# Kernel optimization log

Measured on AMD Instinct MI355X. Metric: run time of the kernel, lower is better.

## Reference

```python
import jax, jax.numpy as jnp
import numpy as np

EPS = 1e-05


def setup_inputs() -> dict:
    key = jax.random.key(0)
    k1, k2, k3, k4 = jax.random.split(key, 4)
    B, C, L, S = 32, 256, 8192, 4
    x = jax.random.normal(k1, (B, C, L), dtype=jnp.float32)
    style_ids = jax.random.randint(k2, (B,), 0, S)
    # per-style affine params, as in nn.InstanceNorm1d(affine=True):
    # torch initializes weight=1, bias=0; use small perturbations so styles differ
    weight = jnp.ones((S, C), dtype=jnp.float32) + 0.1 * jax.random.normal(k3, (S, C), dtype=jnp.float32)
    bias = 0.1 * jax.random.normal(k4, (S, C), dtype=jnp.float32)
    return {"x": x, "weight": weight, "bias": bias, "style_ids": style_ids}


def reference(x, weight, bias, style_ids):
    # x: [B, C, L]; instance norm: normalize each (b, c) row over L (biased var)
    mean = jnp.mean(x, axis=-1, keepdims=True)            # [B, C, 1]
    var = jnp.mean(jnp.square(x - mean), axis=-1, keepdims=True)  # biased, [B, C, 1]
    x_hat = (x - mean) * jax.lax.rsqrt(var + EPS)
    # gather per-sample style affine params: [B, C]
    w = weight[style_ids]
    b = bias[style_ids]
    return x_hat * w[:, :, None] + b[:, :, None]
```

## Files before the change

kernel.cpp:

```cpp
#include <hip/hip_runtime.h>
#include <math.h>


constexpr int L_LEN  = 8192;
constexpr int NTHR   = 512;
constexpr int VPT    = L_LEN / (NTHR * 4);
constexpr int NWAVE  = NTHR / 64;
constexpr float EPS_ = 1e-5f;

typedef float f32x4 __attribute__((ext_vector_type(4)));

__global__ __launch_bounds__(NTHR) void cin1d_kernel(
    const float* __restrict__ x,
    const float* __restrict__ weight,
    const float* __restrict__ bias,
    const int*   __restrict__ style_ids,
    float* __restrict__ out,
    int C)
{
    const int row = blockIdx.x;
    const int b   = row / C;
    const int c   = row - b * C;
    const int t   = threadIdx.x;

    const int   sid = style_ids[b];
    const float w   = weight[sid * C + c];
    const float bb  = bias[sid * C + c];

    const f32x4* __restrict__ xr   = reinterpret_cast<const f32x4*>(x + (size_t)row * L_LEN);
    f32x4* __restrict__       outr = reinterpret_cast<f32x4*>(out + (size_t)row * L_LEN);

    f32x4 v[VPT];
    float sum = 0.f, sq = 0.f;
#pragma unroll
    for (int i = 0; i < VPT; ++i) {
        v[i] = __builtin_nontemporal_load(&xr[t + i * NTHR]);
        sum += v[i].x + v[i].y + v[i].z + v[i].w;
        sq  += v[i].x * v[i].x + v[i].y * v[i].y + v[i].z * v[i].z + v[i].w * v[i].w;
    }

#pragma unroll
    for (int off = 32; off > 0; off >>= 1) {
        sum += __shfl_xor(sum, off, 64);
        sq  += __shfl_xor(sq,  off, 64);
    }

    __shared__ float s_sum[NWAVE];
    __shared__ float s_sq[NWAVE];
    const int wave = t >> 6;
    const int lane = t & 63;
    if (lane == 0) { s_sum[wave] = sum; s_sq[wave] = sq; }
    __syncthreads();

    float ts = 0.f, tq = 0.f;
#pragma unroll
    for (int wv = 0; wv < NWAVE; ++wv) { ts += s_sum[wv]; tq += s_sq[wv]; }
    const float inv_n = 1.0f / (float)L_LEN;
    const float mean  = ts * inv_n;
    const float var   = tq * inv_n - mean * mean;
    const float rstd  = rsqrtf(var + EPS_);
    const float scale = w * rstd;
    const float shift = bb - mean * scale;

#pragma unroll
    for (int i = 0; i < VPT; ++i) {
        f32x4 o;
        o.x = v[i].x * scale + shift;
        o.y = v[i].y * scale + shift;
        o.z = v[i].z * scale + shift;
        o.w = v[i].w * scale + shift;
        __builtin_nontemporal_store(o, &outr[t + i * NTHR]);
    }
}

extern "C" void kernel_launch(void* const* d_in, const int* in_sizes, int n_in,
                              void* d_out, int out_size, void* d_ws, size_t ws_size,
                              hipStream_t stream) {
    const float* x      = (const float*)d_in[0];
    const float* weight = (const float*)d_in[1];
    const float* bias   = (const float*)d_in[2];
    const int*   sids   = (const int*)d_in[3];
    float*       out    = (float*)d_out;

    const int B = in_sizes[3];
    const int C = in_sizes[0] / (B * L_LEN);
    const int rows = B * C;

    cin1d_kernel<<<rows, NTHR, 0, stream>>>(x, weight, bias, sids, out, C);
}
```

Baseline: 96.49 us.

## Process four rows per block with double-buffered prefetch of next row

Each block now handles four consecutive rows instead of one, and loads the next row into a second register buffer while reducing and writing the current row. This aims to hide global load latency behind the reduction, sync and store phases and to cut per-block launch overhead. In exchange it doubles register use per thread, which may lower occupancy, and it reduces the block count fourfold. It assumes C is divisible by 4.

```diff
diff --git a/kernel.cpp b/kernel.cpp
--- a/kernel.cpp
+++ b/kernel.cpp
@@ -2,10 +2,11 @@
 #include <math.h>
 
 
-constexpr int L_LEN  = 8192;
-constexpr int NTHR   = 512;
-constexpr int VPT    = L_LEN / (NTHR * 4);
-constexpr int NWAVE  = NTHR / 64;
+constexpr int L_LEN = 8192;
+constexpr int NTHR  = 512;
+constexpr int VPT   = L_LEN / (NTHR * 4);
+constexpr int NWAVE = NTHR / 64;
+constexpr int RPB   = 4;
 constexpr float EPS_ = 1e-5f;
 
 typedef float f32x4 __attribute__((ext_vector_type(4)));
@@ -18,58 +19,81 @@
     float* __restrict__ out,
     int C)
 {
-    const int row = blockIdx.x;
-    const int b   = row / C;
-    const int c   = row - b * C;
-    const int t   = threadIdx.x;
+    const int row0 = blockIdx.x * RPB;
+    const int b    = row0 / C;
+    const int c0   = row0 - b * C;
+    const int t    = threadIdx.x;
+    const int wave = t >> 6;
+    const int lane = t & 63;
 
-    const int   sid = style_ids[b];
-    const float w   = weight[sid * C + c];
-    const float bb  = bias[sid * C + c];
-
-    const f32x4* __restrict__ xr   = reinterpret_cast<const f32x4*>(x + (size_t)row * L_LEN);
-    f32x4* __restrict__       outr = reinterpret_cast<f32x4*>(out + (size_t)row * L_LEN);
-
-    f32x4 v[VPT];
-    float sum = 0.f, sq = 0.f;
+    const int sid = style_ids[b];
+    float w_[RPB], bb_[RPB];
 #pragma unroll
-    for (int i = 0; i < VPT; ++i) {
-        v[i] = __builtin_nontemporal_load(&xr[t + i * NTHR]);
-        sum += v[i].x + v[i].y + v[i].z + v[i].w;
-        sq  += v[i].x * v[i].x + v[i].y * v[i].y + v[i].z * v[i].z + v[i].w * v[i].w;
+    for (int r = 0; r < RPB; ++r) {
+        w_[r]  = weight[sid * C + c0 + r];
+        bb_[r] = bias[sid * C + c0 + r];
     }
 
-#pragma unroll
-    for (int off = 32; off > 0; off >>= 1) {
-        sum += __shfl_xor(sum, off, 64);
-        sq  += __shfl_xor(sq,  off, 64);
-    }
+    constexpr int ROWV = L_LEN / 4;
+    const f32x4* __restrict__ xr   = reinterpret_cast<const f32x4*>(x   + (size_t)row0 * L_LEN);
+    f32x4* __restrict__       outr = reinterpret_cast<f32x4*>(out + (size_t)row0 * L_LEN);
 
-    __shared__ float s_sum[NWAVE];
-    __shared__ float s_sq[NWAVE];
-    const int wave = t >> 6;
-    const int lane = t & 63;
-    if (lane == 0) { s_sum[wave] = sum; s_sq[wave] = sq; }
-    __syncthreads();
+    __shared__ float s_sum[RPB][NWAVE];
+    __shared__ float s_sq[RPB][NWAVE];
 
-    float ts = 0.f, tq = 0.f;
-#pragma unroll
-    for (int wv = 0; wv < NWAVE; ++wv) { ts += s_sum[wv]; tq += s_sq[wv]; }
-    const float inv_n = 1.0f / (float)L_LEN;
-    const float mean  = ts * inv_n;
-    const float var   = tq * inv_n - mean * mean;
-    const float rstd  = rsqrtf(var + EPS_);
-    const float scale = w * rstd;
-    const float shift = bb - mean * scale;
+    f32x4 buf[2][VPT];
 
 #pragma unroll
-    for (int i = 0; i < VPT; ++i) {
-        f32x4 o;
-        o.x = v[i].x * scale + shift;
-        o.y = v[i].y * scale + shift;
-        o.z = v[i].z * scale + shift;
-        o.w = v[i].w * scale + shift;
-        __builtin_nontemporal_store(o, &outr[t + i * NTHR]);
+    for (int i = 0; i < VPT; ++i)
+        buf[0][i] = __builtin_nontemporal_load(&xr[t + i * NTHR]);
+
+#pragma unroll
+    for (int r = 0; r < RPB; ++r) {
+        const int cur = r & 1;
+
+        if (r + 1 < RPB) {
+#pragma unroll
+            for (int i = 0; i < VPT; ++i)
+                buf[cur ^ 1][i] = __builtin_nontemporal_load(&xr[(r + 1) * ROWV + t + i * NTHR]);
+        }
+
+        float sum = 0.f, sq = 0.f;
+#pragma unroll
+        for (int i = 0; i < VPT; ++i) {
+            const f32x4 v = buf[cur][i];
+            sum += v.x + v.y + v.z + v.w;
+            sq  += v.x * v.x + v.y * v.y + v.z * v.z + v.w * v.w;
+        }
+
+#pragma unroll
+        for (int off = 32; off > 0; off >>= 1) {
+            sum += __shfl_xor(sum, off, 64);
+            sq  += __shfl_xor(sq,  off, 64);
+        }
+
+        if (lane == 0) { s_sum[r][wave] = sum; s_sq[r][wave] = sq; }
+        __syncthreads();
+
+        float ts = 0.f, tq = 0.f;
+#pragma unroll
+        for (int wv = 0; wv < NWAVE; ++wv) { ts += s_sum[r][wv]; tq += s_sq[r][wv]; }
+        const float inv_n = 1.0f / (float)L_LEN;
+        const float mean  = ts * inv_n;
+        const float var   = tq * inv_n - mean * mean;
+        const float rstd  = rsqrtf(var + EPS_);
+        const float scale = w_[r] * rstd;
+        const float shift = bb_[r] - mean * scale;
+
+#pragma unroll
+        for (int i = 0; i < VPT; ++i) {
+            const f32x4 v = buf[cur][i];
+            f32x4 o;
+            o.x = v.x * scale + shift;
+            o.y = v.y * scale + shift;
+            o.z = v.z * scale + shift;
+            o.w = v.w * scale + shift;
+            __builtin_nontemporal_store(o, &outr[r * ROWV + t + i * NTHR]);
+        }
     }
 }
 
@@ -85,6 +109,7 @@
     const int B = in_sizes[3];
     const int C = in_sizes[0] / (B * L_LEN);
     const int rows = B * C;
+    const int blocks = rows / RPB;
 
-    cin1d_kernel<<<rows, NTHR, 0, stream>>>(x, weight, bias, sids, out, C);
+    cin1d_kernel<<<blocks, NTHR, 0, stream>>>(x, weight, bias, sids, out, C);
 }
```

After: 98.58 us. +2.2%, slower.
